# Optimization experiments

Measured on AMD Instinct MI355X. Metric: run time of the kernel, lower is better.

Reference implementation:

```python
import jax, jax.numpy as jnp
import numpy as np

B, S, F = 4, 2048, 512
H, DK, DV, FILT = 8, 64, 64, 512

def setup_inputs() -> dict:
    key = jax.random.key(0)
    ks = jax.random.split(key, 11)
    sc_in = 1.0 / np.sqrt(F)
    sc_o = 1.0 / np.sqrt(H * DV)
    return {
        "x_q": jax.random.normal(ks[0], (B, S, F), jnp.float32),
        "x_k": jax.random.normal(ks[1], (B, S, F), jnp.float32),
        "x_v": jax.random.normal(ks[2], (B, S, F), jnp.float32),
        "Wq": jax.random.normal(ks[3], (H, F, DK), jnp.float32) * sc_in,
        "bq": jax.random.normal(ks[4], (H, DK), jnp.float32) * 0.01,
        "Wk": jax.random.normal(ks[5], (H, F, DK), jnp.float32) * sc_in,
        "bk": jax.random.normal(ks[6], (H, DK), jnp.float32) * 0.01,
        "Wv": jax.random.normal(ks[7], (H, F, DV), jnp.float32) * sc_in,
        "bv": jax.random.normal(ks[8], (H, DV), jnp.float32) * 0.01,
        "Wo": jax.random.normal(ks[9], (H * DV, FILT), jnp.float32) * sc_o,
        "bo": jax.random.normal(ks[10], (FILT,), jnp.float32) * 0.01,
    }

def reference(x_q, x_k, x_v, Wq, bq, Wk, bk, Wv, bv, Wo, bo):
    d_k = Wq.shape[-1]
    # per-head Dense projections, batched over heads: [B,H,S,dk/dv]
    q = jnp.einsum("bsf,hfk->bhsk", x_q, Wq) + bq[:, None, :]
    k = jnp.einsum("bsf,hfk->bhsk", x_k, Wk) + bk[:, None, :]
    v = jnp.einsum("bsf,hfv->bhsv", x_v, Wv) + bv[:, None, :]
    # scaled dot-product attention (scale by 1/sqrt(d_k) as in map_fn)
    scores = jnp.einsum("bhsk,bhtk->bhst", q, k) / jnp.sqrt(jnp.asarray(d_k, q.dtype))
    attn = jax.nn.softmax(scores, axis=-1)
    out = jnp.einsum("bhst,bhtv->bhsv", attn, v)
    # concat heads along feature dim -> [B,S,H*DV], then output linear
    bsz, h, s, dv = out.shape
    concat = out.transpose(0, 2, 1, 3).reshape(bsz, s, h * dv)
    return concat @ Wo + bo
```

## Files before the change

### kernel.cpp

```cpp
#include <hip/hip_runtime.h>

#define B_    4
#define S_    2048
#define H_    8
#define M_    (B_ * S_)

typedef __bf16    bf16_t;
typedef _Float16  f16_t;
typedef __bf16   bf16x8 __attribute__((ext_vector_type(8)));
typedef __bf16   bf16x4 __attribute__((ext_vector_type(4)));
typedef _Float16 f16x8  __attribute__((ext_vector_type(8)));
typedef float    f32x16 __attribute__((ext_vector_type(16)));

union B8 { uint4 u; bf16x8 v; bf16_t e[8]; };
union B4 { uint2 u; bf16x4 v; bf16_t e[4]; };
union H8 { uint4 u; f16x8  v; f16_t  e[8]; };
union H4 { uint2 u; f16_t  e[4]; };

#define QSCALE 0.1803368801111204f

typedef const __attribute__((address_space(1))) unsigned int ga_u32;
typedef __attribute__((address_space(3))) unsigned int       ls_u32;
__device__ __forceinline__ void g2l16(const void* g, void* l) {
    __builtin_amdgcn_global_load_lds((ga_u32*)g, (ls_u32*)l, 16, 0, 0);
}

__global__ __launch_bounds__(256) void prep(
    const float* __restrict__ xq, const float* __restrict__ xk,
    const float* __restrict__ xv,
    bf16_t* __restrict__ dq, bf16_t* __restrict__ dk, bf16_t* __restrict__ dv,
    const float* __restrict__ w0, const float* __restrict__ w1,
    const float* __restrict__ w2, const float* __restrict__ wo,
    bf16_t* __restrict__ t0, bf16_t* __restrict__ t1,
    bf16_t* __restrict__ t2, f16_t* __restrict__ wot)
{
    __shared__ float T[64][65];
    const int bid = blockIdx.x;
    const int tid = threadIdx.x;

    if (bid < 3072) {
        const int z  = bid >> 10;
        const int bx = bid & 1023;
        const float* src = z == 0 ? xq : z == 1 ? xk : xv;
        bf16_t*      dst = z == 0 ? dq : z == 1 ? dk : dv;
        const size_t base = (size_t)bx * 4096 + tid * 8;
        #pragma unroll
        for (int k = 0; k < 2; ++k) {
            const size_t i = base + (size_t)k * 2048;
            float4 a = *(const float4*)(src + i);
            float4 b = *(const float4*)(src + i + 4);
            B8 o;
            o.e[0] = (bf16_t)a.x; o.e[1] = (bf16_t)a.y;
            o.e[2] = (bf16_t)a.z; o.e[3] = (bf16_t)a.w;
            o.e[4] = (bf16_t)b.x; o.e[5] = (bf16_t)b.y;
            o.e[6] = (bf16_t)b.z; o.e[7] = (bf16_t)b.w;
            *(uint4*)(dst + i) = o.u;
        }
        return;
    }

    const int cid = bid - 3072;
    const int z   = cid >> 6;
    const int rem = cid & 63;
    const int k0  = (rem & 7) * 64;
    const int row = tid & 63, q4 = tid >> 6;

    if (z < 3) {
        const float* W  = z == 0 ? w0 : z == 1 ? w1 : w2;
        bf16_t*      Wt = z == 0 ? t0 : z == 1 ? t1 : t2;
        const int h = rem >> 3;
        const float* Wh = W + (size_t)h * 512 * 64;
        #pragma unroll
        for (int i = 0; i < 4; ++i) {
            int fq = q4 * 4 + i;
            float4 v = *(const float4*)(Wh + (size_t)(k0 + row) * 64 + fq * 4);
            T[row][fq * 4 + 0] = v.x; T[row][fq * 4 + 1] = v.y;
            T[row][fq * 4 + 2] = v.z; T[row][fq * 4 + 3] = v.w;
        }
        __syncthreads();
        bf16_t* Wth = Wt + (size_t)h * 64 * 512;
        #pragma unroll
        for (int i = 0; i < 4; ++i) {
            int kq = q4 * 4 + i;
            B4 o;
            #pragma unroll
            for (int j = 0; j < 4; ++j) o.e[j] = (bf16_t)T[kq * 4 + j][row];
            *(uint2*)(Wth + (size_t)row * 512 + k0 + kq * 4) = o.u;
        }
    } else {
        const int n0 = (rem >> 3) * 64;
        #pragma unroll
        for (int i = 0; i < 4; ++i) {
            int fq = q4 * 4 + i;
            float4 v = *(const float4*)(wo + (size_t)(k0 + row) * 512 + n0 + fq * 4);
            T[row][fq * 4 + 0] = v.x; T[row][fq * 4 + 1] = v.y;
            T[row][fq * 4 + 2] = v.z; T[row][fq * 4 + 3] = v.w;
        }
        __syncthreads();
        #pragma unroll
        for (int i = 0; i < 4; ++i) {
            int kq = q4 * 4 + i;
            H4 o;
            #pragma unroll
            for (int j = 0; j < 4; ++j) o.e[j] = (f16_t)T[kq * 4 + j][row];
            *(uint2*)(wot + (size_t)(n0 + row) * 512 + k0 + kq * 4) = o.u;
        }
    }
}

__global__ __launch_bounds__(256) void proj_tiled(
    const bf16_t* __restrict__ xq, const bf16_t* __restrict__ xk,
    const bf16_t* __restrict__ xv,
    const bf16_t* __restrict__ Wtq, const bf16_t* __restrict__ Wtk,
    const bf16_t* __restrict__ Wtv,
    const float* __restrict__ bq, const float* __restrict__ bk,
    const float* __restrict__ bv,
    bf16_t* __restrict__ Qb, bf16_t* __restrict__ Kb, bf16_t* __restrict__ Vt)
{
    __shared__ char sm[34816];
    bf16_t* As = (bf16_t*)sm;
    bf16_t* Bs = As + 128 * 64;

    const int z = blockIdx.z;
    const bf16_t* X    = z == 0 ? xq  : z == 1 ? xk  : xv;
    const bf16_t* Wt   = z == 0 ? Wtq : z == 1 ? Wtk : Wtv;
    const float*  bias = z == 0 ? bq  : z == 1 ? bk  : bv;

    const int tid  = threadIdx.x;
    const int wave = tid >> 6, lane = tid & 63;
    const int l31  = lane & 31, half = lane >> 5;
    const int m0   = blockIdx.x * 128;
    const int n0   = blockIdx.y * 128;
    const int mw   = (wave & 1) * 64;
    const int nw   = (wave >> 1) * 64;

    const int srow = lane >> 3;
    const int scol = (lane & 7) * 16;

    f32x16 acc[2][2];
    #pragma unroll
    for (int mt = 0; mt < 2; ++mt)
        #pragma unroll
        for (int nt = 0; nt < 2; ++nt)
            #pragma unroll
            for (int i = 0; i < 16; ++i) acc[mt][nt][i] = 0.0f;

    for (int k0 = 0; k0 < 512; k0 += 64) {
        __syncthreads();
        #pragma unroll
        for (int i = 0; i < 4; ++i) {
            const int inst = wave * 4 + i;
            const int row  = inst * 8 + srow;
            g2l16((const char*)X  + ((size_t)(m0 + row) * 512 + k0) * 2 + scol,
                  sm + inst * 1024);
            g2l16((const char*)Wt + ((size_t)(n0 + row) * 512 + k0) * 2 + scol,
                  sm + 16384 + inst * 1024);
        }
        __syncthreads();

        #pragma unroll
        for (int kc = 0; kc < 4; ++kc) {
            B8 a0, a1, b0, b1;
            a0.u = *(const uint4*)&As[(mw + l31)      * 64 + kc * 16 + half * 8];
            a1.u = *(const uint4*)&As[(mw + 32 + l31) * 64 + kc * 16 + half * 8];
            b0.u = *(const uint4*)&Bs[(nw + l31)      * 64 + kc * 16 + half * 8];
            b1.u = *(const uint4*)&Bs[(nw + 32 + l31) * 64 + kc * 16 + half * 8];
            acc[0][0] = __builtin_amdgcn_mfma_f32_32x32x16_bf16(a0.v, b0.v, acc[0][0], 0, 0, 0);
            acc[0][1] = __builtin_amdgcn_mfma_f32_32x32x16_bf16(a0.v, b1.v, acc[0][1], 0, 0, 0);
            acc[1][0] = __builtin_amdgcn_mfma_f32_32x32x16_bf16(a1.v, b0.v, acc[1][0], 0, 0, 0);
            acc[1][1] = __builtin_amdgcn_mfma_f32_32x32x16_bf16(a1.v, b1.v, acc[1][1], 0, 0, 0);
        }
    }

    if (z <= 1) {
        const float sc_ = (z == 0) ? QSCALE : 1.0f;
        bf16_t* Out = (z == 0) ? Qb : Kb;
        #pragma unroll
        for (int mt = 0; mt < 2; ++mt)
            #pragma unroll
            for (int nt = 0; nt < 2; ++nt) {
                int n = n0 + nw + nt * 32 + l31;
                float bv_ = bias[n];
                #pragma unroll
                for (int r = 0; r < 16; ++r) {
                    int m = m0 + mw + mt * 32 + (r & 3) + 8 * (r >> 2) + 4 * half;
                    Out[(size_t)m * 512 + n] = (bf16_t)((acc[mt][nt][r] + bv_) * sc_);
                }
            }
    } else {
        const int b  = m0 >> 11;
        const int sb = m0 & 2047;
        __syncthreads();
        #pragma unroll
        for (int mt = 0; mt < 2; ++mt)
            #pragma unroll
            for (int nt = 0; nt < 2; ++nt) {
                const int nl  = nw + nt * 32 + l31;
                const float bv_ = bias[n0 + nl];
                #pragma unroll
                for (int r = 0; r < 16; r += 2) {
                    const int ml = mw + mt * 32 + (r & 3) + 8 * (r >> 2) + 4 * half;
                    union { unsigned u; bf16_t e[2]; } pk;
                    pk.e[0] = (bf16_t)(acc[mt][nt][r]     + bv_);
                    pk.e[1] = (bf16_t)(acc[mt][nt][r + 1] + bv_);
                    *(unsigned*)(sm + nl * 272 + ml * 2) = pk.u;
                }
            }
        __syncthreads();
        const int dl16 = tid >> 4;
        const int cc   = tid & 15;
        #pragma unroll
        for (int p = 0; p < 8; ++p) {
            const int d_l = p * 16 + dl16;
            const int ng  = n0 + d_l;
            const int h   = ng >> 6, dd = ng & 63;
            uint4 val = *(const uint4*)(sm + d_l * 272 + cc * 16);
            *(uint4*)(Vt + ((size_t)((b * 8 + h) * 64 + dd)) * 2048 + sb + cc * 8) = val;
        }
    }
}

__global__ __launch_bounds__(512, 2) void attn_mfma(
    const bf16_t* __restrict__ Q, const bf16_t* __restrict__ K,
    const bf16_t* __restrict__ Vt, f16_t* __restrict__ O)
{
    __shared__ char smraw[71680];
    bf16_t* KsBuf = (bf16_t*)smraw;
    bf16_t* VsBuf = KsBuf + 2 * 64 * 72;

    const int bh  = blockIdx.y;
    const int b   = bh >> 3, h = bh & 7;
    const int q0  = blockIdx.x * 256;
    const int tid = threadIdx.x;
    const int wave = tid >> 6, lane = tid & 63;
    const int l31 = lane & 31, half = lane >> 5;
    const int qsub = wave & 3, ksplit = wave >> 2;

    bf16x8 qfA[4], qfB[4];
    {
        const bf16_t* qp = Q + ((size_t)(b * S_ + q0 + qsub * 64 + l31)) * 512 + h * 64 + half * 8;
        #pragma unroll
        for (int ks = 0; ks < 4; ++ks) {
            B8 t;
            t.u = *(const uint4*)(qp + ks * 16);              qfA[ks] = t.v;
            t.u = *(const uint4*)(qp + 32 * 512 + ks * 16);   qfB[ks] = t.v;
        }
    }

    f32x16 oA0, oA1, oB0, oB1;
    #pragma unroll
    for (int i = 0; i < 16; ++i) { oA0[i] = 0.0f; oA1[i] = 0.0f; oB0[i] = 0.0f; oB1[i] = 0.0f; }
    float lA = 0.0f, lB = 0.0f;

    const bf16_t* Kbase = K + ((size_t)b * S_) * 512 + h * 64;
    const bf16_t* Vbase = Vt + ((size_t)bh * 64) * 2048;

    const int sbuf = tid >> 8;
    const int p    = tid & 255;
    const int kr = p >> 3, kc8 = p & 7;
    const int vd = p >> 2, vj = p & 3;
    const int kqmap[4] = {0, 2, 1, 3};
    const int vkq = kqmap[vj];
    bf16_t* KsS = KsBuf + sbuf * (64 * 72);
    bf16_t* VsS = VsBuf + sbuf * (64 * 72);
    const bf16_t* KsC = KsBuf + ksplit * (64 * 72);
    const bf16_t* VsC = VsBuf + ksplit * (64 * 72);

    uint4 kreg0, kreg1;
    uint2 vreg[4];
    {
        const int tb = sbuf * 1024;
        kreg0 = *(const uint4*)(Kbase + (size_t)(tb + kr) * 512 + kc8 * 8);
        kreg1 = *(const uint4*)(Kbase + (size_t)(tb + kr + 32) * 512 + kc8 * 8);
        #pragma unroll
        for (int g = 0; g < 4; ++g)
            vreg[g] = *(const uint2*)(Vbase + (size_t)vd * 2048 + tb + g * 16 + vkq * 4);
    }

    for (int t0 = 0; t0 < 1024; t0 += 64) {
        __syncthreads();
        *(uint4*)&KsS[kr * 72 + kc8 * 8]        = kreg0;
        *(uint4*)&KsS[(kr + 32) * 72 + kc8 * 8] = kreg1;
        #pragma unroll
        for (int g = 0; g < 4; ++g)
            *(uint2*)&VsS[vd * 72 + g * 16 + vj * 4] = vreg[g];
        __syncthreads();

        if (t0 + 64 < 1024) {
            const int tb = sbuf * 1024 + t0 + 64;
            kreg0 = *(const uint4*)(Kbase + (size_t)(tb + kr) * 512 + kc8 * 8);
            kreg1 = *(const uint4*)(Kbase + (size_t)(tb + kr + 32) * 512 + kc8 * 8);
            #pragma unroll
            for (int g = 0; g < 4; ++g)
                vreg[g] = *(const uint2*)(Vbase + (size_t)vd * 2048 + tb + g * 16 + vkq * 4);
        }

        f32x16 s00, s01, s10, s11;
        #pragma unroll
        for (int i = 0; i < 16; ++i) { s00[i] = 0.0f; s01[i] = 0.0f; s10[i] = 0.0f; s11[i] = 0.0f; }
        #pragma unroll
        for (int ks = 0; ks < 4; ++ks) {
            B8 kk0, kk1;
            kk0.u = *(const uint4*)(&KsC[l31 * 72 + ks * 16 + half * 8]);
            kk1.u = *(const uint4*)(&KsC[(32 + l31) * 72 + ks * 16 + half * 8]);
            s00 = __builtin_amdgcn_mfma_f32_32x32x16_bf16(kk0.v, qfA[ks], s00, 0, 0, 0);
            s01 = __builtin_amdgcn_mfma_f32_32x32x16_bf16(kk0.v, qfB[ks], s01, 0, 0, 0);
            s10 = __builtin_amdgcn_mfma_f32_32x32x16_bf16(kk1.v, qfA[ks], s10, 0, 0, 0);
            s11 = __builtin_amdgcn_mfma_f32_32x32x16_bf16(kk1.v, qfB[ks], s11, 0, 0, 0);
        }

        float lsA = 0.0f, lsB = 0.0f;
        #pragma unroll
        for (int r = 0; r < 16; ++r) {
            s00[r] = __builtin_amdgcn_exp2f(s00[r]); lsA += s00[r];
            s10[r] = __builtin_amdgcn_exp2f(s10[r]); lsA += s10[r];
            s01[r] = __builtin_amdgcn_exp2f(s01[r]); lsB += s01[r];
            s11[r] = __builtin_amdgcn_exp2f(s11[r]); lsB += s11[r];
        }
        lA += lsA; lB += lsB;

        B8 pfA[4], pfB[4];
        #pragma unroll
        for (int j = 0; j < 8; ++j) {
            pfA[0].e[j] = (bf16_t)s00[j];
            pfA[1].e[j] = (bf16_t)s00[8 + j];
            pfA[2].e[j] = (bf16_t)s10[j];
            pfA[3].e[j] = (bf16_t)s10[8 + j];
            pfB[0].e[j] = (bf16_t)s01[j];
            pfB[1].e[j] = (bf16_t)s01[8 + j];
            pfB[2].e[j] = (bf16_t)s11[j];
            pfB[3].e[j] = (bf16_t)s11[8 + j];
        }

        #pragma unroll
        for (int c = 0; c < 4; ++c) {
            B8 va, vb;
            va.u = *(const uint4*)(&VsC[l31 * 72 + c * 16 + half * 8]);
            vb.u = *(const uint4*)(&VsC[(32 + l31) * 72 + c * 16 + half * 8]);
            oA0 = __builtin_amdgcn_mfma_f32_32x32x16_bf16(va.v, pfA[c].v, oA0, 0, 0, 0);
            oA1 = __builtin_amdgcn_mfma_f32_32x32x16_bf16(vb.v, pfA[c].v, oA1, 0, 0, 0);
            oB0 = __builtin_amdgcn_mfma_f32_32x32x16_bf16(va.v, pfB[c].v, oB0, 0, 0, 0);
            oB1 = __builtin_amdgcn_mfma_f32_32x32x16_bf16(vb.v, pfB[c].v, oB1, 0, 0, 0);
        }
    }

    lA += __shfl_xor(lA, 32);
    lB += __shfl_xor(lB, 32);
    __syncthreads();
    float* co = (float*)smraw;
    float* cl = co + 4 * 64 * 68;
    if (ksplit == 1) {
        float* reg = co + qsub * (64 * 68);
        #pragma unroll
        for (int r = 0; r < 16; ++r) {
            reg[r * 68 + lane]        = oA0[r];
            reg[(16 + r) * 68 + lane] = oA1[r];
            reg[(32 + r) * 68 + lane] = oB0[r];
            reg[(48 + r) * 68 + lane] = oB1[r];
        }
        cl[qsub * 128 + lane]      = lA;
        cl[qsub * 128 + 64 + lane] = lB;
    }
    __syncthreads();
    if (ksplit == 0) {
        float* reg = co + qsub * (64 * 68);
        float invA = 1.0f / (lA + cl[qsub * 128 + lane]);
        float invB = 1.0f / (lB + cl[qsub * 128 + 64 + lane]);
        f16_t* ObA = O + ((size_t)(b * S_ + q0 + qsub * 64 + l31)) * 512 + h * 64;
        f16_t* ObB = ObA + (size_t)32 * 512;
        #pragma unroll
        for (int g = 0; g < 4; ++g) {
            H4 a, c, e, f;
            #pragma unroll
            for (int j = 0; j < 4; ++j) {
                int r = g * 4 + j;
                a.e[j] = (f16_t)((oA0[r] + reg[r * 68 + lane])        * invA);
                c.e[j] = (f16_t)((oA1[r] + reg[(16 + r) * 68 + lane]) * invA);
                e.e[j] = (f16_t)((oB0[r] + reg[(32 + r) * 68 + lane]) * invB);
                f.e[j] = (f16_t)((oB1[r] + reg[(48 + r) * 68 + lane]) * invB);
            }
            int d = 8 * g + 4 * half;
            *(uint2*)(ObA + d)      = a.u;
            *(uint2*)(ObA + 32 + d) = c.u;
            *(uint2*)(ObB + d)      = e.u;
            *(uint2*)(ObB + 32 + d) = f.u;
        }
    }
}

__global__ __launch_bounds__(256) void gemm_out_tiled(
    const f16_t* __restrict__ A, const f16_t* __restrict__ Wot,
    const float* __restrict__ bias, float* __restrict__ C)
{
    __shared__ f16_t As[64 * 72];
    __shared__ f16_t Bs[64 * 72];

    const int tid  = threadIdx.x;
    const int wave = tid >> 6, lane = tid & 63;
    const int l31  = lane & 31, half = lane >> 5;
    const int m0   = blockIdx.x * 64;
    const int n0   = blockIdx.y * 64;
    const int mw   = (wave & 1) * 32;
    const int nw   = (wave >> 1) * 32;

    const int sr  = tid >> 2;
    const int so  = (tid & 3) * 16;

    uint4 pA0, pA1, pB0, pB1;
    {
        const f16_t* ap = A   + (size_t)(m0 + sr) * 512 + so;
        const f16_t* bp = Wot + (size_t)(n0 + sr) * 512 + so;
        pA0 = *(const uint4*)(ap); pA1 = *(const uint4*)(ap + 8);
        pB0 = *(const uint4*)(bp); pB1 = *(const uint4*)(bp + 8);
    }

    f32x16 acc;
    #pragma unroll
    for (int i = 0; i < 16; ++i) acc[i] = 0.0f;

    for (int k0 = 0; k0 < 512; k0 += 64) {
        __syncthreads();
        *(uint4*)&As[sr * 72 + so]     = pA0;
        *(uint4*)&As[sr * 72 + so + 8] = pA1;
        *(uint4*)&Bs[sr * 72 + so]     = pB0;
        *(uint4*)&Bs[sr * 72 + so + 8] = pB1;
        __syncthreads();
        if (k0 + 64 < 512) {
            const f16_t* ap = A   + (size_t)(m0 + sr) * 512 + k0 + 64 + so;
            const f16_t* bp = Wot + (size_t)(n0 + sr) * 512 + k0 + 64 + so;
            pA0 = *(const uint4*)(ap); pA1 = *(const uint4*)(ap + 8);
            pB0 = *(const uint4*)(bp); pB1 = *(const uint4*)(bp + 8);
        }

        #pragma unroll
        for (int kc = 0; kc < 4; ++kc) {
            H8 a, b;
            a.u = *(const uint4*)&As[(mw + l31) * 72 + kc * 16 + half * 8];
            b.u = *(const uint4*)&Bs[(nw + l31) * 72 + kc * 16 + half * 8];
            acc = __builtin_amdgcn_mfma_f32_32x32x16_f16(a.v, b.v, acc, 0, 0, 0);
        }
    }

    const int n = n0 + nw + l31;
    const float bias0 = bias[n];
    #pragma unroll
    for (int r = 0; r < 16; ++r) {
        int m = m0 + mw + (r & 3) + 8 * (r >> 2) + 4 * half;
        C[(size_t)m * 512 + n] = acc[r] + bias0;
    }
}

extern "C" void kernel_launch(void* const* d_in, const int* in_sizes, int n_in,
                              void* d_out, int out_size, void* d_ws, size_t ws_size,
                              hipStream_t stream)
{
    const float* x_q = (const float*)d_in[0];
    const float* x_k = (const float*)d_in[1];
    const float* x_v = (const float*)d_in[2];
    const float* Wq  = (const float*)d_in[3];
    const float* bq  = (const float*)d_in[4];
    const float* Wk  = (const float*)d_in[5];
    const float* bk  = (const float*)d_in[6];
    const float* Wv  = (const float*)d_in[7];
    const float* bv  = (const float*)d_in[8];
    const float* Wo  = (const float*)d_in[9];
    const float* bo  = (const float*)d_in[10];
    float* out = (float*)d_out;

    char* W = (char*)d_ws;
    bf16_t* Wtq = (bf16_t*)W;
    bf16_t* Wtk = Wtq + (size_t)8 * 64 * 512;
    bf16_t* Wtv = Wtk + (size_t)8 * 64 * 512;
    f16_t*  Wot = (f16_t*)(Wtv + (size_t)8 * 64 * 512);
    bf16_t* Qb  = (bf16_t*)(Wot + (size_t)512 * 512);
    bf16_t* Kb  = Qb + (size_t)M_ * 512;
    bf16_t* Vt  = Kb + (size_t)M_ * 512;
    f16_t*  AO  = (f16_t*)(Vt + (size_t)M_ * 512);

    bf16_t* Xqb = (bf16_t*)out;
    bf16_t* Xkb = Xqb + (size_t)M_ * 512;
    bf16_t* Xvb = (bf16_t*)AO;

    prep<<<dim3(3328), 256, 0, stream>>>(
        x_q, x_k, x_v, Xqb, Xkb, Xvb,
        Wq, Wk, Wv, Wo, Wtq, Wtk, Wtv, Wot);

    proj_tiled<<<dim3(64, 4, 3), 256, 0, stream>>>(
        Xqb, Xkb, Xvb, Wtq, Wtk, Wtv, bq, bk, bv, Qb, Kb, Vt);

    attn_mfma<<<dim3(S_ / 256, B_ * H_), 512, 0, stream>>>(Qb, Kb, Vt, AO);

    gemm_out_tiled<<<dim3(128, 8), 256, 0, stream>>>(AO, Wot, bo, out);
}
```

Baseline: 191.7 us.

## Load K/V tiles directly from global into registers and remap blocks per XCD

```diff
diff --git a/kernel.cpp b/kernel.cpp
--- a/kernel.cpp
+++ b/kernel.cpp
@@ -225,12 +225,12 @@
     const bf16_t* __restrict__ Vt, f16_t* __restrict__ O)
 {
     __shared__ char smraw[71680];
-    bf16_t* KsBuf = (bf16_t*)smraw;
-    bf16_t* VsBuf = KsBuf + 2 * 64 * 72;
-
-    const int bh  = blockIdx.y;
+
+    const int lin = (int)(blockIdx.x + gridDim.x * blockIdx.y);
+    const int xcd = lin & 7, sl = lin >> 3;
+    const int bh  = xcd * 4 + (sl >> 3);
+    const int q0  = (sl & 7) * 256;
     const int b   = bh >> 3, h = bh & 7;
-    const int q0  = blockIdx.x * 256;
     const int tid = threadIdx.x;
     const int wave = tid >> 6, lane = tid & 63;
     const int l31 = lane & 31, half = lane >> 5;
@@ -255,44 +255,17 @@
     const bf16_t* Kbase = K + ((size_t)b * S_) * 512 + h * 64;
     const bf16_t* Vbase = Vt + ((size_t)bh * 64) * 2048;
 
-    const int sbuf = tid >> 8;
-    const int p    = tid & 255;
-    const int kr = p >> 3, kc8 = p & 7;
-    const int vd = p >> 2, vj = p & 3;
-    const int kqmap[4] = {0, 2, 1, 3};
-    const int vkq = kqmap[vj];
-    bf16_t* KsS = KsBuf + sbuf * (64 * 72);
-    bf16_t* VsS = VsBuf + sbuf * (64 * 72);
-    const bf16_t* KsC = KsBuf + ksplit * (64 * 72);
-    const bf16_t* VsC = VsBuf + ksplit * (64 * 72);
-
-    uint4 kreg0, kreg1;
-    uint2 vreg[4];
-    {
-        const int tb = sbuf * 1024;
-        kreg0 = *(const uint4*)(Kbase + (size_t)(tb + kr) * 512 + kc8 * 8);
-        kreg1 = *(const uint4*)(Kbase + (size_t)(tb + kr + 32) * 512 + kc8 * 8);
-        #pragma unroll
-        for (int g = 0; g < 4; ++g)
-            vreg[g] = *(const uint2*)(Vbase + (size_t)vd * 2048 + tb + g * 16 + vkq * 4);
-    }
+    const bf16_t* kp0 = Kbase + (size_t)(ksplit * 1024 + l31) * 512 + half * 8;
+    const bf16_t* kp1 = kp0 + (size_t)32 * 512;
+    const bf16_t* vp0 = Vbase + (size_t)l31 * 2048 + ksplit * 1024 + half * 4;
+    const bf16_t* vp1 = vp0 + (size_t)32 * 2048;
 
     for (int t0 = 0; t0 < 1024; t0 += 64) {
-        __syncthreads();
-        *(uint4*)&KsS[kr * 72 + kc8 * 8]        = kreg0;
-        *(uint4*)&KsS[(kr + 32) * 72 + kc8 * 8] = kreg1;
-        #pragma unroll
-        for (int g = 0; g < 4; ++g)
-            *(uint2*)&VsS[vd * 72 + g * 16 + vj * 4] = vreg[g];
-        __syncthreads();
-
-        if (t0 + 64 < 1024) {
-            const int tb = sbuf * 1024 + t0 + 64;
-            kreg0 = *(const uint4*)(Kbase + (size_t)(tb + kr) * 512 + kc8 * 8);
-            kreg1 = *(const uint4*)(Kbase + (size_t)(tb + kr + 32) * 512 + kc8 * 8);
-            #pragma unroll
-            for (int g = 0; g < 4; ++g)
-                vreg[g] = *(const uint2*)(Vbase + (size_t)vd * 2048 + tb + g * 16 + vkq * 4);
+        B8 kk0[4], kk1[4];
+        #pragma unroll
+        for (int ks = 0; ks < 4; ++ks) {
+            kk0[ks].u = *(const uint4*)(kp0 + t0 * 512 + ks * 16);
+            kk1[ks].u = *(const uint4*)(kp1 + t0 * 512 + ks * 16);
         }
 
         f32x16 s00, s01, s10, s11;
@@ -300,13 +273,19 @@
         for (int i = 0; i < 16; ++i) { s00[i] = 0.0f; s01[i] = 0.0f; s10[i] = 0.0f; s11[i] = 0.0f; }
         #pragma unroll
         for (int ks = 0; ks < 4; ++ks) {
-            B8 kk0, kk1;
-            kk0.u = *(const uint4*)(&KsC[l31 * 72 + ks * 16 + half * 8]);
-            kk1.u = *(const uint4*)(&KsC[(32 + l31) * 72 + ks * 16 + half * 8]);
-            s00 = __builtin_amdgcn_mfma_f32_32x32x16_bf16(kk0.v, qfA[ks], s00, 0, 0, 0);
-            s01 = __builtin_amdgcn_mfma_f32_32x32x16_bf16(kk0.v, qfB[ks], s01, 0, 0, 0);
-            s10 = __builtin_amdgcn_mfma_f32_32x32x16_bf16(kk1.v, qfA[ks], s10, 0, 0, 0);
-            s11 = __builtin_amdgcn_mfma_f32_32x32x16_bf16(kk1.v, qfB[ks], s11, 0, 0, 0);
+            s00 = __builtin_amdgcn_mfma_f32_32x32x16_bf16(kk0[ks].v, qfA[ks], s00, 0, 0, 0);
+            s01 = __builtin_amdgcn_mfma_f32_32x32x16_bf16(kk0[ks].v, qfB[ks], s01, 0, 0, 0);
+            s10 = __builtin_amdgcn_mfma_f32_32x32x16_bf16(kk1[ks].v, qfA[ks], s10, 0, 0, 0);
+            s11 = __builtin_amdgcn_mfma_f32_32x32x16_bf16(kk1[ks].v, qfB[ks], s11, 0, 0, 0);
+        }
+
+        B8 va[4], vb[4];
+        #pragma unroll
+        for (int c = 0; c < 4; ++c) {
+            *(uint2*)&va[c].e[0] = *(const uint2*)(vp0 + t0 + c * 16);
+            *(uint2*)&va[c].e[4] = *(const uint2*)(vp0 + t0 + c * 16 + 8);
+            *(uint2*)&vb[c].e[0] = *(const uint2*)(vp1 + t0 + c * 16);
+            *(uint2*)&vb[c].e[4] = *(const uint2*)(vp1 + t0 + c * 16 + 8);
         }
 
         float lsA = 0.0f, lsB = 0.0f;
@@ -334,13 +313,10 @@
 
         #pragma unroll
         for (int c = 0; c < 4; ++c) {
-            B8 va, vb;
-            va.u = *(const uint4*)(&VsC[l31 * 72 + c * 16 + half * 8]);
-            vb.u = *(const uint4*)(&VsC[(32 + l31) * 72 + c * 16 + half * 8]);
-            oA0 = __builtin_amdgcn_mfma_f32_32x32x16_bf16(va.v, pfA[c].v, oA0, 0, 0, 0);
-            oA1 = __builtin_amdgcn_mfma_f32_32x32x16_bf16(vb.v, pfA[c].v, oA1, 0, 0, 0);
-            oB0 = __builtin_amdgcn_mfma_f32_32x32x16_bf16(va.v, pfB[c].v, oB0, 0, 0, 0);
-            oB1 = __builtin_amdgcn_mfma_f32_32x32x16_bf16(vb.v, pfB[c].v, oB1, 0, 0, 0);
+            oA0 = __builtin_amdgcn_mfma_f32_32x32x16_bf16(va[c].v, pfA[c].v, oA0, 0, 0, 0);
+            oA1 = __builtin_amdgcn_mfma_f32_32x32x16_bf16(vb[c].v, pfA[c].v, oA1, 0, 0, 0);
+            oB0 = __builtin_amdgcn_mfma_f32_32x32x16_bf16(va[c].v, pfB[c].v, oB0, 0, 0, 0);
+            oB1 = __builtin_amdgcn_mfma_f32_32x32x16_bf16(vb[c].v, pfB[c].v, oB1, 0, 0, 0);
         }
     }
 
@@ -488,7 +464,7 @@
     proj_tiled<<<dim3(64, 4, 3), 256, 0, stream>>>(
         Xqb, Xkb, Xvb, Wtq, Wtk, Wtv, bq, bk, bv, Qb, Kb, Vt);
 
-    attn_mfma<<<dim3(S_ / 256, B_ * H_), 512, 0, stream>>>(Qb, Kb, Vt, AO);
+    attn_mfma<<<dim3(8, 32), 512, 0, stream>>>(Qb, Kb, Vt, AO);
 
     gemm_out_tiled<<<dim3(128, 8), 256, 0, stream>>>(AO, Wot, bo, out);
 }
```

Result: slower. 245.8 us (+28.2%).

## Double-buffer K/V LDS tiles to use one barrier per iteration

Applied to the files above, without the earlier changes.

```diff
diff --git a/kernel.cpp b/kernel.cpp
--- a/kernel.cpp
+++ b/kernel.cpp
@@ -224,9 +224,9 @@
     const bf16_t* __restrict__ Q, const bf16_t* __restrict__ K,
     const bf16_t* __restrict__ Vt, f16_t* __restrict__ O)
 {
-    __shared__ char smraw[71680];
-    bf16_t* KsBuf = (bf16_t*)smraw;
-    bf16_t* VsBuf = KsBuf + 2 * 64 * 72;
+    __shared__ char smraw[73728];
+    bf16_t* Ks = (bf16_t*)smraw;
+    bf16_t* Vs = Ks + 4 * 64 * 72;
 
     const int bh  = blockIdx.y;
     const int b   = bh >> 3, h = bh & 7;
@@ -261,39 +261,40 @@
     const int vd = p >> 2, vj = p & 3;
     const int kqmap[4] = {0, 2, 1, 3};
     const int vkq = kqmap[vj];
-    bf16_t* KsS = KsBuf + sbuf * (64 * 72);
-    bf16_t* VsS = VsBuf + sbuf * (64 * 72);
-    const bf16_t* KsC = KsBuf + ksplit * (64 * 72);
-    const bf16_t* VsC = VsBuf + ksplit * (64 * 72);
 
     uint4 kreg0, kreg1;
     uint2 vreg[4];
-    {
-        const int tb = sbuf * 1024;
-        kreg0 = *(const uint4*)(Kbase + (size_t)(tb + kr) * 512 + kc8 * 8);
-        kreg1 = *(const uint4*)(Kbase + (size_t)(tb + kr + 32) * 512 + kc8 * 8);
-        #pragma unroll
-        for (int g = 0; g < 4; ++g)
-            vreg[g] = *(const uint2*)(Vbase + (size_t)vd * 2048 + tb + g * 16 + vkq * 4);
-    }
-
-    for (int t0 = 0; t0 < 1024; t0 += 64) {
-        __syncthreads();
-        *(uint4*)&KsS[kr * 72 + kc8 * 8]        = kreg0;
-        *(uint4*)&KsS[(kr + 32) * 72 + kc8 * 8] = kreg1;
-        #pragma unroll
-        for (int g = 0; g < 4; ++g)
-            *(uint2*)&VsS[vd * 72 + g * 16 + vj * 4] = vreg[g];
-        __syncthreads();
-
-        if (t0 + 64 < 1024) {
-            const int tb = sbuf * 1024 + t0 + 64;
-            kreg0 = *(const uint4*)(Kbase + (size_t)(tb + kr) * 512 + kc8 * 8);
-            kreg1 = *(const uint4*)(Kbase + (size_t)(tb + kr + 32) * 512 + kc8 * 8);
-            #pragma unroll
-            for (int g = 0; g < 4; ++g)
-                vreg[g] = *(const uint2*)(Vbase + (size_t)vd * 2048 + tb + g * 16 + vkq * 4);
-        }
+
+#define LOADSET(TB) do {                                                      \
+        kreg0 = *(const uint4*)(Kbase + (size_t)((TB) + kr) * 512 + kc8 * 8); \
+        kreg1 = *(const uint4*)(Kbase + (size_t)((TB) + kr + 32) * 512 + kc8 * 8); \
+        _Pragma("unroll")                                                     \
+        for (int g = 0; g < 4; ++g)                                           \
+            vreg[g] = *(const uint2*)(Vbase + (size_t)vd * 2048 + (TB) + g * 16 + vkq * 4); \
+    } while (0)
+
+#define WRITESET(SLOT) do {                                                   \
+        bf16_t* KsS = Ks + ((SLOT) * 2 + sbuf) * 4608;                        \
+        bf16_t* VsS = Vs + ((SLOT) * 2 + sbuf) * 4608;                        \
+        *(uint4*)&KsS[kr * 72 + kc8 * 8]        = kreg0;                      \
+        *(uint4*)&KsS[(kr + 32) * 72 + kc8 * 8] = kreg1;                      \
+        _Pragma("unroll")                                                     \
+        for (int g = 0; g < 4; ++g)                                           \
+            *(uint2*)&VsS[vd * 72 + g * 16 + vj * 4] = vreg[g];               \
+    } while (0)
+
+    LOADSET(sbuf * 1024);
+    WRITESET(0);
+    LOADSET(sbuf * 1024 + 64);
+    __syncthreads();
+
+    for (int it = 0; it < 16; ++it) {
+        const int slot = it & 1;
+        if (it + 1 < 16) WRITESET(slot ^ 1);
+        if (it + 2 < 16) LOADSET(sbuf * 1024 + (it + 2) * 64);
+
+        const bf16_t* KsC = Ks + (slot * 2 + ksplit) * 4608;
+        const bf16_t* VsC = Vs + (slot * 2 + ksplit) * 4608;
 
         f32x16 s00, s01, s10, s11;
         #pragma unroll
@@ -342,7 +343,11 @@
             oB0 = __builtin_amdgcn_mfma_f32_32x32x16_bf16(va.v, pfB[c].v, oB0, 0, 0, 0);
             oB1 = __builtin_amdgcn_mfma_f32_32x32x16_bf16(vb.v, pfB[c].v, oB1, 0, 0, 0);
         }
-    }
+
+        __syncthreads();
+    }
+#undef LOADSET
+#undef WRITESET
 
     lA += __shfl_xor(lA, 32);
     lB += __shfl_xor(lB, 32);
```

New measurement: 201.0 us. +4.9%, slower.
